# Optimization experiments

Hardware: AMD Instinct MI355X
Metric: run time of the kernel (lower is better)

Reference implementation:

```python
import jax, jax.numpy as jnp
import numpy as np

EMBED_DIM = 1024
NUM_HEADS = 16
HEAD_DIM = EMBED_DIM // NUM_HEADS


def setup_inputs() -> dict:
    key = jax.random.key(0)
    ks = jax.random.split(key, 8)
    B, S, D = 2, 2048, EMBED_DIM
    scale = 1.0 / np.sqrt(D)
    return {
        "query": jax.random.normal(ks[0], (B, S, D), dtype=jnp.float32),
        "key": jax.random.normal(ks[1], (B, S, D), dtype=jnp.float32),
        "value": jax.random.normal(ks[2], (B, S, D), dtype=jnp.float32),
        "Wq": jax.random.normal(ks[3], (D, D), dtype=jnp.float32) * scale,
        "Wk": jax.random.normal(ks[4], (D, D), dtype=jnp.float32) * scale,
        "Wv": jax.random.normal(ks[5], (D, D), dtype=jnp.float32) * scale,
        "Wo": jax.random.normal(ks[6], (D, D), dtype=jnp.float32) * scale,
        "attention_mask": jax.random.randint(ks[7], (B, S), 0, 2, dtype=jnp.int32),
    }


def reference(query, key, value, Wq, Wk, Wv, Wo, attention_mask):
    B, Sq, D = query.shape
    Sk = key.shape[1]
    H, hd = NUM_HEADS, HEAD_DIM
    # linear projections (no bias), split into heads: [B, H, S, hd]
    q = (query @ Wq).reshape(B, Sq, H, hd).transpose(0, 2, 1, 3)
    k = (key @ Wk).reshape(B, Sk, H, hd).transpose(0, 2, 1, 3)
    v = (value @ Wv).reshape(B, Sk, H, hd).transpose(0, 2, 1, 3)
    # scaled dot-product scores: [B, H, Sq, Sk]; scale uses head_dim (post-split key dim)
    scores = jnp.einsum("bhqd,bhkd->bhqk", q, k) / jnp.sqrt(jnp.float32(hd))
    # padding mask [B, Sk] broadcast to [B, 1, 1, Sk]; 0 -> -inf
    mask = attention_mask[:, None, None, :]
    scores = jnp.where(mask == 0, -jnp.inf, scores)
    weights = jax.nn.softmax(scores, axis=-1)
    out = jnp.einsum("bhqk,bhkd->bhqd", weights, v)  # [B, H, Sq, hd]
    out = out.transpose(0, 2, 1, 3).reshape(B, Sq, D)
    return out @ Wo
```

## Files before the change

### kernel.cpp

```cpp
#include <hip/hip_runtime.h>
#include <hip/hip_bf16.h>

typedef short bf16x8 __attribute__((ext_vector_type(8)));
typedef float f32x4 __attribute__((ext_vector_type(4)));

#define S_LEN 2048
#define NHEAD 16
#define DM 1024

#if __has_builtin(__builtin_amdgcn_exp2f)
#define EXP2(x) __builtin_amdgcn_exp2f(x)
#else
#define EXP2(x) exp2f(x)
#endif

__device__ __forceinline__ short f2bf(float f) {
  union { float f; unsigned u; } x; x.f = f;
  unsigned r = x.u + 0x7fffu + ((x.u >> 16) & 1u);
  return (short)(r >> 16);
}

__device__ __forceinline__ void gload16(const void* g, void* l) {
  __builtin_amdgcn_global_load_lds(
      (const __attribute__((address_space(1))) void*)g,
      (__attribute__((address_space(3))) void*)l, 16, 0, 0);
}

__global__ __launch_bounds__(256) void wtrans(const float* __restrict__ Wq, const float* __restrict__ Wk,
                                              const float* __restrict__ Wv, const float* __restrict__ Wo,
                                              short* Tq, short* Tk, short* Tv, short* To) {
  const int z = blockIdx.z;
  const float* W = (z == 0) ? Wq : (z == 1) ? Wk : (z == 2) ? Wv : Wo;
  short* T = (z == 0) ? Tq : (z == 1) ? Tk : (z == 2) ? Tv : To;
  __shared__ short Tl[64][72];
  const int tid = threadIdx.x;
  const int k0 = blockIdx.x * 64, n0 = blockIdx.y * 64;
  const int r = tid >> 2, c0 = (tid & 3) * 16;
#pragma unroll
  for (int j = 0; j < 4; j++) {
    float4 v = *(const float4*)&W[(size_t)(k0 + r) * DM + n0 + c0 + 4 * j];
    Tl[r][c0 + 4 * j + 0] = f2bf(v.x);
    Tl[r][c0 + 4 * j + 1] = f2bf(v.y);
    Tl[r][c0 + 4 * j + 2] = f2bf(v.z);
    Tl[r][c0 + 4 * j + 3] = f2bf(v.w);
  }
  __syncthreads();
  bf16x8 o0, o1;
#pragma unroll
  for (int j = 0; j < 8; j++) { o0[j] = Tl[c0 + j][r]; o1[j] = Tl[c0 + 8 + j][r]; }
  *(bf16x8*)&T[(size_t)(n0 + r) * DM + k0 + c0] = o0;
  *(bf16x8*)&T[(size_t)(n0 + r) * DM + k0 + c0 + 8] = o1;
}

__global__ __launch_bounds__(256) void xcvt(const float* __restrict__ q, const float* __restrict__ k,
                                            const float* __restrict__ v,
                                            short* xq, short* xk, short* xv) {
  const int z = blockIdx.y;
  const float* src = (z == 0) ? q : (z == 1) ? k : v;
  short* dst = (z == 0) ? xq : (z == 1) ? xk : xv;
  const size_t base = ((size_t)blockIdx.x * 256 + threadIdx.x) * 16;
  float4 a = *(const float4*)&src[base];
  float4 b = *(const float4*)&src[base + 4];
  float4 c = *(const float4*)&src[base + 8];
  float4 d = *(const float4*)&src[base + 12];
  bf16x8 o0, o1;
  o0[0] = f2bf(a.x); o0[1] = f2bf(a.y); o0[2] = f2bf(a.z); o0[3] = f2bf(a.w);
  o0[4] = f2bf(b.x); o0[5] = f2bf(b.y); o0[6] = f2bf(b.z); o0[7] = f2bf(b.w);
  o1[0] = f2bf(c.x); o1[1] = f2bf(c.y); o1[2] = f2bf(c.z); o1[3] = f2bf(c.w);
  o1[4] = f2bf(d.x); o1[5] = f2bf(d.y); o1[6] = f2bf(d.z); o1[7] = f2bf(d.w);
  *(bf16x8*)&dst[base] = o0;
  *(bf16x8*)&dst[base + 8] = o1;
}

template<int CM>
__global__ __launch_bounds__(256) void gemm3(const short* __restrict__ A, const short* __restrict__ Bt,
                                             void* __restrict__ Cp, int M, int N, int K) {
  __shared__ __align__(16) short Al[2][128 * 64];
  __shared__ __align__(16) short Bl[2][64 * 64];
  const int tid = threadIdx.x;
  const int lane = tid & 63, w = tid >> 6;
  const int wm = w >> 1, wn = w & 1;
  const int lr = lane & 15, g = lane >> 4;
  const int m0 = blockIdx.y * 128, n0 = blockIdx.x * 64;

  f32x4 acc[4][2];
#pragma unroll
  for (int i = 0; i < 4; i++)
#pragma unroll
    for (int j = 0; j < 2; j++) acc[i][j] = (f32x4){0.f, 0.f, 0.f, 0.f};

  const int srow = lane >> 3;
  const int sch = (lane & 7) ^ (srow & 7);
  const short* gA = A + (size_t)(m0 + w * 32 + srow) * K + 8 * sch;
  const short* gB = Bt + (size_t)(n0 + w * 16 + srow) * K + 8 * sch;

#define STAGE(buf, kk)                                                              \
  do {                                                                              \
    _Pragma("unroll") for (int c = 0; c < 4; c++)                                   \
        gload16(gA + (size_t)c * 8 * K + (kk), &Al[buf][(w * 32 + c * 8) * 64]);    \
    _Pragma("unroll") for (int c = 0; c < 2; c++)                                   \
        gload16(gB + (size_t)c * 8 * K + (kk), &Bl[buf][(w * 16 + c * 8) * 64]);    \
  } while (0)

  const int nsteps = K >> 6;
  STAGE(0, 0);
  int buf = 0;
  for (int t = 0; t < nsteps; t++) {
    __syncthreads();
    if (t + 1 < nsteps) STAGE(buf ^ 1, (t + 1) << 6);
#pragma unroll
    for (int kc = 0; kc < 2; kc++) {
      bf16x8 af[4], bfr[2];
#pragma unroll
      for (int mt = 0; mt < 4; mt++) {
        int row = wm * 64 + mt * 16 + lr;
        af[mt] = *(const bf16x8*)&Al[buf][row * 64 + 8 * ((kc * 4 + g) ^ (lr & 7))];
      }
#pragma unroll
      for (int nt = 0; nt < 2; nt++) {
        int row = wn * 32 + nt * 16 + lr;
        bfr[nt] = *(const bf16x8*)&Bl[buf][row * 64 + 8 * ((kc * 4 + g) ^ (lr & 7))];
      }
      __builtin_amdgcn_s_setprio(1);
#pragma unroll
      for (int mt = 0; mt < 4; mt++)
#pragma unroll
        for (int nt = 0; nt < 2; nt++)
          acc[mt][nt] = __builtin_amdgcn_mfma_f32_16x16x32_bf16(af[mt], bfr[nt], acc[mt][nt], 0, 0, 0);
      __builtin_amdgcn_s_setprio(0);
    }
    buf ^= 1;
  }
#undef STAGE

#pragma unroll
  for (int mt = 0; mt < 4; mt++)
#pragma unroll
    for (int nt = 0; nt < 2; nt++)
#pragma unroll
      for (int r = 0; r < 4; r++) {
        int row = m0 + wm * 64 + mt * 16 + g * 4 + r;
        int col = n0 + wn * 32 + nt * 16 + lr;
        if (CM == 0) {
          ((float*)Cp)[(size_t)row * N + col] = acc[mt][nt][r];
        } else if (CM == 1 || CM == 3) {
          float v = (CM == 3) ? acc[mt][nt][r] * 0.18033688011f : acc[mt][nt][r];
          int b = row >> 11, s = row & (S_LEN - 1);
          int h = col >> 6, d = col & 63;
          ((short*)Cp)[(((size_t)(b * NHEAD + h)) * S_LEN + s) * 64 + d] = f2bf(v);
        } else {
          int h = row >> 6, d = row & 63;
          int b = col >> 11, s = col & (S_LEN - 1);
          ((short*)Cp)[(((size_t)(b * NHEAD + h)) * 64 + d) * S_LEN + s] = f2bf(acc[mt][nt][r]);
        }
      }
}

template<int AM, int BMODE, int CM>
__global__ __launch_bounds__(256) void gemm2(const void* __restrict__ Ap, const void* __restrict__ Bp,
                                             void* __restrict__ Cp, int M, int N, int K) {
  __shared__ __align__(16) short Al[128][72];
  __shared__ __align__(16) short Bl[64][72];
  const int tid = threadIdx.x;
  const int lane = tid & 63, w = tid >> 6;
  const int wm = w >> 1, wn = w & 1;
  const int lr = lane & 15, g = lane >> 4;
  const int m0 = blockIdx.y * 128, n0 = blockIdx.x * 64;

  f32x4 acc[4][2];
#pragma unroll
  for (int i = 0; i < 4; i++)
#pragma unroll
    for (int j = 0; j < 2; j++) acc[i][j] = (f32x4){0.f, 0.f, 0.f, 0.f};

  const int ar = tid >> 1, ac = (tid & 1) * 32;
  const int br = tid >> 2, bc = (tid & 3) * 16;

  float4 la[8]; bf16x8 la8[4];
  float4 lb[4]; bf16x8 lb8[2];

#define LOADA(kk)                                                                        \
  do {                                                                                   \
    if (AM == 0) {                                                                       \
      const float* A = (const float*)Ap;                                                 \
      _Pragma("unroll") for (int j = 0; j < 8; j++)                                      \
          la[j] = *(const float4*)&A[(size_t)(m0 + ar) * K + (kk) + ac + 4 * j];         \
    } else {                                                                             \
      const short* A = (const short*)Ap;                                                 \
      _Pragma("unroll") for (int j = 0; j < 4; j++)                                      \
          la8[j] = *(const bf16x8*)&A[(size_t)(m0 + ar) * K + (kk) + ac + 8 * j];        \
    }                                                                                    \
  } while (0)

#define LOADB(kk)                                                                        \
  do {                                                                                   \
    if (BMODE == 0) {                                                                    \
      const float* B = (const float*)Bp;                                                 \
      _Pragma("unroll") for (int j = 0; j < 4; j++)                                      \
          lb[j] = *(const float4*)&B[(size_t)(n0 + br) * K + (kk) + bc + 4 * j];         \
    } else if (BMODE == 1) {                                                             \
      const short* B = (const short*)Bp;                                                 \
      _Pragma("unroll") for (int j = 0; j < 2; j++)                                      \
          lb8[j] = *(const bf16x8*)&B[(size_t)(n0 + br) * K + (kk) + bc + 8 * j];        \
    } else {                                                                             \
      const float* B = (const float*)Bp;                                                 \
      _Pragma("unroll") for (int j = 0; j < 4; j++)                                      \
          lb[j] = *(const float4*)&B[(size_t)((kk) + br) * N + n0 + bc + 4 * j];         \
    }                                                                                    \
  } while (0)

  const int nsteps = K >> 6;
  LOADA(0); LOADB(0);

  for (int t = 0; t < nsteps; t++) {
    __syncthreads();
    if (AM == 0) {
#pragma unroll
      for (int j = 0; j < 4; j++) {
        float4 v0 = la[2 * j], v1 = la[2 * j + 1];
        bf16x8 tt;
        tt[0] = f2bf(v0.x); tt[1] = f2bf(v0.y); tt[2] = f2bf(v0.z); tt[3] = f2bf(v0.w);
        tt[4] = f2bf(v1.x); tt[5] = f2bf(v1.y); tt[6] = f2bf(v1.z); tt[7] = f2bf(v1.w);
        *(bf16x8*)&Al[ar][ac + 8 * j] = tt;
      }
    } else {
#pragma unroll
      for (int j = 0; j < 4; j++) *(bf16x8*)&Al[ar][ac + 8 * j] = la8[j];
    }
    if (BMODE == 0) {
#pragma unroll
      for (int j = 0; j < 2; j++) {
        float4 v0 = lb[2 * j], v1 = lb[2 * j + 1];
        bf16x8 tt;
        tt[0] = f2bf(v0.x); tt[1] = f2bf(v0.y); tt[2] = f2bf(v0.z); tt[3] = f2bf(v0.w);
        tt[4] = f2bf(v1.x); tt[5] = f2bf(v1.y); tt[6] = f2bf(v1.z); tt[7] = f2bf(v1.w);
        *(bf16x8*)&Bl[br][bc + 8 * j] = tt;
      }
    } else if (BMODE == 1) {
#pragma unroll
      for (int j = 0; j < 2; j++) *(bf16x8*)&Bl[br][bc + 8 * j] = lb8[j];
    } else {
#pragma unroll
      for (int j = 0; j < 4; j++) {
        float4 v = lb[j];
        Bl[bc + 4 * j + 0][br] = f2bf(v.x);
        Bl[bc + 4 * j + 1][br] = f2bf(v.y);
        Bl[bc + 4 * j + 2][br] = f2bf(v.z);
        Bl[bc + 4 * j + 3][br] = f2bf(v.w);
      }
    }
    __syncthreads();
    if (t + 1 < nsteps) { LOADA((t + 1) << 6); LOADB((t + 1) << 6); }
#pragma unroll
    for (int kc = 0; kc < 2; kc++) {
      bf16x8 af[4], bfr[2];
#pragma unroll
      for (int mt = 0; mt < 4; mt++) af[mt] = *(const bf16x8*)&Al[wm * 64 + mt * 16 + lr][kc * 32 + g * 8];
#pragma unroll
      for (int nt = 0; nt < 2; nt++) bfr[nt] = *(const bf16x8*)&Bl[wn * 32 + nt * 16 + lr][kc * 32 + g * 8];
#pragma unroll
      for (int mt = 0; mt < 4; mt++)
#pragma unroll
        for (int nt = 0; nt < 2; nt++)
          acc[mt][nt] = __builtin_amdgcn_mfma_f32_16x16x32_bf16(af[mt], bfr[nt], acc[mt][nt], 0, 0, 0);
    }
  }
#undef LOADA
#undef LOADB

#pragma unroll
  for (int mt = 0; mt < 4; mt++)
#pragma unroll
    for (int nt = 0; nt < 2; nt++)
#pragma unroll
      for (int r = 0; r < 4; r++) {
        int row = m0 + wm * 64 + mt * 16 + g * 4 + r;
        int col = n0 + wn * 32 + nt * 16 + lr;
        if (CM == 0) {
          ((float*)Cp)[(size_t)row * N + col] = acc[mt][nt][r];
        } else if (CM == 1 || CM == 3) {
          float v = (CM == 3) ? acc[mt][nt][r] * 0.18033688011f : acc[mt][nt][r];
          int b = row >> 11, s = row & (S_LEN - 1);
          int h = col >> 6, d = col & 63;
          ((short*)Cp)[(((size_t)(b * NHEAD + h)) * S_LEN + s) * 64 + d] = f2bf(v);
        } else {
          int h = row >> 6, d = row & 63;
          int b = col >> 11, s = col & (S_LEN - 1);
          ((short*)Cp)[(((size_t)(b * NHEAD + h)) * 64 + d) * S_LEN + s] = f2bf(acc[mt][nt][r]);
        }
      }
}

__global__ __launch_bounds__(256, 2) void attn4(const short* __restrict__ Qb,
                                                const short* __restrict__ Kb,
                                                const short* __restrict__ VbT,
                                                const int* __restrict__ mask,
                                                short* __restrict__ Ob) {
  __shared__ __align__(16) short Kl[2][64][64];
  __shared__ __align__(16) short Vl[2][64][64];
  __shared__ __align__(16) short Pl[4][32][64];

  const int tid = threadIdx.x;
  const int lane = tid & 63, w = tid >> 6;
  const int lr = lane & 15, g = lane >> 4;

  const int flat = blockIdx.y * gridDim.x + blockIdx.x;
  const int wid = (flat & 7) * 64 + (flat >> 3);
  const int qblk = wid & 15, bh = wid >> 4;
  const int b = bh >> 4, h = bh & 15;
  const int qbase = qblk * 128;
  const size_t hoff = (size_t)bh * S_LEN * 64;

  bf16x8 qf[2][2];
#pragma unroll
  for (int qfr = 0; qfr < 2; qfr++)
#pragma unroll
    for (int kh = 0; kh < 2; kh++)
      qf[qfr][kh] = *(const bf16x8*)&Qb[hoff + (size_t)(qbase + w * 32 + qfr * 16 + lr) * 64 + kh * 32 + g * 8];

  f32x4 o_acc[2][4];
  float lsum[2][4];
#pragma unroll
  for (int qfr = 0; qfr < 2; qfr++) {
#pragma unroll
    for (int dg = 0; dg < 4; dg++) o_acc[qfr][dg] = (f32x4){0.f, 0.f, 0.f, 0.f};
#pragma unroll
    for (int r = 0; r < 4; r++) lsum[qfr][r] = 0.f;
  }

  const int* maskb = mask + b * S_LEN;
  const int srow = lane >> 3;
  const int sch = (lane & 7) ^ (srow & 7);
  const short* gK = Kb + hoff + (size_t)(w * 16 + srow) * 64 + 8 * sch;
  const short* gV = VbT + hoff + (size_t)(w * 16 + srow) * S_LEN + 8 * sch;

#define STAGEKV(buf, kb)                                                       \
  do {                                                                         \
    _Pragma("unroll") for (int c = 0; c < 2; c++)                              \
        gload16(gK + (size_t)(kb + c * 8) * 64, &Kl[buf][w * 16 + c * 8][0]);  \
    _Pragma("unroll") for (int c = 0; c < 2; c++)                              \
        gload16(gV + (size_t)c * 8 * S_LEN + (kb), &Vl[buf][w * 16 + c * 8][0]); \
  } while (0)

  const int NT = S_LEN / 64;
  STAGEKV(0, 0);
  int buf = 0;

  for (int t = 0; t < NT; t++) {
    const int kb = t * 64;
    __syncthreads();
    if (t + 1 < NT) STAGEKV(buf ^ 1, kb + 64);

    float bias[4];
#pragma unroll
    for (int nt = 0; nt < 4; nt++) bias[nt] = maskb[kb + 16 * nt + lr] ? 0.f : -1e30f;

    bf16x8 kfr[4][2];
#pragma unroll
    for (int nt = 0; nt < 4; nt++)
#pragma unroll
      for (int kh = 0; kh < 2; kh++)
        kfr[nt][kh] = *(const bf16x8*)&Kl[buf][nt * 16 + lr][8 * ((4 * kh + g) ^ (lr & 7))];

    f32x4 s[2][4];
#pragma unroll
    for (int qfr = 0; qfr < 2; qfr++)
#pragma unroll
      for (int nt = 0; nt < 4; nt++) s[qfr][nt] = (f32x4){0.f, 0.f, 0.f, 0.f};
    __builtin_amdgcn_s_setprio(1);
#pragma unroll
    for (int qfr = 0; qfr < 2; qfr++)
#pragma unroll
      for (int nt = 0; nt < 4; nt++) {
        s[qfr][nt] = __builtin_amdgcn_mfma_f32_16x16x32_bf16(qf[qfr][0], kfr[nt][0], s[qfr][nt], 0, 0, 0);
        s[qfr][nt] = __builtin_amdgcn_mfma_f32_16x16x32_bf16(qf[qfr][1], kfr[nt][1], s[qfr][nt], 0, 0, 0);
      }
    __builtin_amdgcn_s_setprio(0);

    bf16x8 vfr[4][2];
#pragma unroll
    for (int dg = 0; dg < 4; dg++)
#pragma unroll
      for (int kh = 0; kh < 2; kh++)
        vfr[dg][kh] = *(const bf16x8*)&Vl[buf][dg * 16 + lr][8 * ((4 * kh + g) ^ (lr & 7))];

#pragma unroll
    for (int qfr = 0; qfr < 2; qfr++)
#pragma unroll
      for (int nt = 0; nt < 4; nt++)
#pragma unroll
        for (int r = 0; r < 4; r++) {
          float p = EXP2(s[qfr][nt][r] + bias[nt]);
          lsum[qfr][r] += p;
          union { float f; unsigned u; } cv; cv.f = p;
          unsigned short pb = (unsigned short)((cv.u + 0x7fffu) >> 16);
          int q = qfr * 16 + g * 4 + r;
          Pl[w][q][(16 * nt + lr) ^ ((q & 7) << 3)] = (short)pb;
        }

#pragma unroll
    for (int qfr = 0; qfr < 2; qfr++) {
      bf16x8 pf[2];
#pragma unroll
      for (int kh = 0; kh < 2; kh++)
        pf[kh] = *(const bf16x8*)&Pl[w][qfr * 16 + lr][8 * ((4 * kh + g) ^ (lr & 7))];
      __builtin_amdgcn_s_setprio(1);
#pragma unroll
      for (int dg = 0; dg < 4; dg++) {
        o_acc[qfr][dg] = __builtin_amdgcn_mfma_f32_16x16x32_bf16(pf[0], vfr[dg][0], o_acc[qfr][dg], 0, 0, 0);
        o_acc[qfr][dg] = __builtin_amdgcn_mfma_f32_16x16x32_bf16(pf[1], vfr[dg][1], o_acc[qfr][dg], 0, 0, 0);
      }
      __builtin_amdgcn_s_setprio(0);
    }
    buf ^= 1;
  }
#undef STAGEKV

#pragma unroll
  for (int qfr = 0; qfr < 2; qfr++)
#pragma unroll
    for (int r = 0; r < 4; r++) {
      float l = lsum[qfr][r];
#pragma unroll
      for (int off = 1; off < 16; off <<= 1) l += __shfl_xor(l, off);
      float inv = 1.f / l;
      int qr = qbase + w * 32 + qfr * 16 + g * 4 + r;
#pragma unroll
      for (int dg = 0; dg < 4; dg++) {
        int col = h * 64 + dg * 16 + lr;
        Ob[((size_t)b * S_LEN + qr) * DM + col] = f2bf(o_acc[qfr][dg][r] * inv);
      }
    }
}

extern "C" void kernel_launch(void* const* d_in, const int* in_sizes, int n_in,
                              void* d_out, int out_size, void* d_ws, size_t ws_size,
                              hipStream_t stream) {
  const float* query = (const float*)d_in[0];
  const float* key   = (const float*)d_in[1];
  const float* value = (const float*)d_in[2];
  const float* Wq = (const float*)d_in[3];
  const float* Wk = (const float*)d_in[4];
  const float* Wv = (const float*)d_in[5];
  const float* Wo = (const float*)d_in[6];
  const int* mask = (const int*)d_in[7];

  char* ws = (char*)d_ws;
  const size_t MB = 1 << 20;
  const bool big = ws_size >= 41 * MB;

  dim3 ag(S_LEN / 128, 2 * NHEAD);

  if (big) {
    short* xq  = (short*)(ws);
    short* xk  = (short*)(ws + 8 * MB);
    short* xv  = (short*)(ws + 16 * MB);
    short* WqT = (short*)(ws + 24 * MB);
    short* WkT = (short*)(ws + 26 * MB);
    short* WvT = (short*)(ws + 28 * MB);
    short* WoT = (short*)(ws + 30 * MB);
    short* Qb  = (short*)(ws + 32 * MB);
    short* Kb  = xq;
    short* VbT = xk;
    short* Ob  = xv;

    dim3 tgrid(16, 16, 4);
    wtrans<<<tgrid, 256, 0, stream>>>(Wq, Wk, Wv, Wo, WqT, WkT, WvT, WoT);
    dim3 cg(1024, 3);
    xcvt<<<cg, 256, 0, stream>>>(query, key, value, xq, xk, xv);

    dim3 gqk(DM / 64, (2 * S_LEN) / 128);
    gemm3<3><<<gqk, 256, 0, stream>>>(xq, WqT, Qb, 2 * S_LEN, DM, DM);
    gemm3<1><<<gqk, 256, 0, stream>>>(xk, WkT, Kb, 2 * S_LEN, DM, DM);
    dim3 gv((2 * S_LEN) / 64, DM / 128);
    gemm3<2><<<gv, 256, 0, stream>>>(WvT, xv, VbT, DM, 2 * S_LEN, DM);

    attn4<<<ag, 256, 0, stream>>>(Qb, Kb, VbT, mask, Ob);

    gemm3<0><<<gqk, 256, 0, stream>>>(Ob, WoT, (float*)d_out, 2 * S_LEN, DM, DM);
  } else {
    short* Qb  = (short*)(ws);
    short* Kb  = (short*)(ws + 8 * MB);
    short* VbT = (short*)(ws + 16 * MB);
    short* WqT = (short*)(ws + 24 * MB);
    short* WkT = (short*)(ws + 26 * MB);
    short* WvT = (short*)(ws + 28 * MB);
    short* Ob  = (short*)(ws + 24 * MB);

    dim3 tgrid(16, 16, 3);
    wtrans<<<tgrid, 256, 0, stream>>>(Wq, Wk, Wv, Wo, WqT, WkT, WvT, WqT);

    dim3 gq(DM / 64, (2 * S_LEN) / 128);
    gemm2<0, 1, 3><<<gq, 256, 0, stream>>>(query, WqT, Qb, 2 * S_LEN, DM, DM);
    gemm2<0, 1, 1><<<gq, 256, 0, stream>>>(key,   WkT, Kb, 2 * S_LEN, DM, DM);
    dim3 gv((2 * S_LEN) / 64, DM / 128);
    gemm2<1, 0, 2><<<gv, 256, 0, stream>>>(WvT, value, VbT, DM, 2 * S_LEN, DM);

    attn4<<<ag, 256, 0, stream>>>(Qb, Kb, VbT, mask, Ob);

    gemm2<1, 2, 0><<<gq, 256, 0, stream>>>(Ob, Wo, (float*)d_out, 2 * S_LEN, DM, DM);
  }
}
```

Before: 146.1 us.

## Enlarge attention query tile to 256 rows and compute transposed scores

The attention kernel now handles 256 query rows per block (64 per wave) instead of 128, so each K/V tile staged in shared memory is reused across twice as many queries, and the grid halves. Scores are computed as K·Qᵀ, which puts each lane's four accumulator values along the key dimension. That lets the softmax numerators be packed into bf16 pairs with a single hardware convert and written to LDS as 8-byte stores, with the mask read as int4 vectors. The row-sum reduction shrinks to two shuffles. In exchange the kernel uses more registers and LDS and drops the 2-blocks-per-CU launch bound, so occupancy may fall and there are only 256 blocks to fill the device.

```diff
diff --git a/kernel.cpp b/kernel.cpp
--- a/kernel.cpp
+++ b/kernel.cpp
@@ -18,6 +18,12 @@
   union { float f; unsigned u; } x; x.f = f;
   unsigned r = x.u + 0x7fffu + ((x.u >> 16) & 1u);
   return (short)(r >> 16);
+}
+
+__device__ __forceinline__ unsigned cvt_pk_bf16(float lo, float hi) {
+  unsigned r;
+  asm("v_cvt_pk_bf16_f32 %0, %1, %2" : "=v"(r) : "v"(lo), "v"(hi));
+  return r;
 }
 
 __device__ __forceinline__ void gload16(const void* g, void* l) {
@@ -291,41 +297,40 @@
       }
 }
 
-__global__ __launch_bounds__(256, 2) void attn4(const short* __restrict__ Qb,
-                                                const short* __restrict__ Kb,
-                                                const short* __restrict__ VbT,
-                                                const int* __restrict__ mask,
-                                                short* __restrict__ Ob) {
+__global__ __launch_bounds__(256) void attn5(const short* __restrict__ Qb,
+                                              const short* __restrict__ Kb,
+                                              const short* __restrict__ VbT,
+                                              const int* __restrict__ mask,
+                                              short* __restrict__ Ob) {
   __shared__ __align__(16) short Kl[2][64][64];
   __shared__ __align__(16) short Vl[2][64][64];
-  __shared__ __align__(16) short Pl[4][32][64];
+  __shared__ __align__(16) short Pl[4][64][64];
 
   const int tid = threadIdx.x;
   const int lane = tid & 63, w = tid >> 6;
   const int lr = lane & 15, g = lane >> 4;
 
   const int flat = blockIdx.y * gridDim.x + blockIdx.x;
-  const int wid = (flat & 7) * 64 + (flat >> 3);
-  const int qblk = wid & 15, bh = wid >> 4;
+  const int wid = (flat & 7) * 32 + (flat >> 3);
+  const int qblk = wid & 7, bh = wid >> 3;
   const int b = bh >> 4, h = bh & 15;
-  const int qbase = qblk * 128;
+  const int qbase = qblk * 256;
   const size_t hoff = (size_t)bh * S_LEN * 64;
 
-  bf16x8 qf[2][2];
-#pragma unroll
-  for (int qfr = 0; qfr < 2; qfr++)
+  bf16x8 qf[4][2];
+#pragma unroll
+  for (int qfr = 0; qfr < 4; qfr++)
 #pragma unroll
     for (int kh = 0; kh < 2; kh++)
-      qf[qfr][kh] = *(const bf16x8*)&Qb[hoff + (size_t)(qbase + w * 32 + qfr * 16 + lr) * 64 + kh * 32 + g * 8];
-
-  f32x4 o_acc[2][4];
-  float lsum[2][4];
-#pragma unroll
-  for (int qfr = 0; qfr < 2; qfr++) {
+      qf[qfr][kh] = *(const bf16x8*)&Qb[hoff + (size_t)(qbase + w * 64 + qfr * 16 + lr) * 64 + kh * 32 + g * 8];
+
+  f32x4 o_acc[4][4];
+  float lsum[4];
+#pragma unroll
+  for (int qfr = 0; qfr < 4; qfr++) {
+    lsum[qfr] = 0.f;
 #pragma unroll
     for (int dg = 0; dg < 4; dg++) o_acc[qfr][dg] = (f32x4){0.f, 0.f, 0.f, 0.f};
-#pragma unroll
-    for (int r = 0; r < 4; r++) lsum[qfr][r] = 0.f;
   }
 
   const int* maskb = mask + b * S_LEN;
@@ -334,11 +339,11 @@
   const short* gK = Kb + hoff + (size_t)(w * 16 + srow) * 64 + 8 * sch;
   const short* gV = VbT + hoff + (size_t)(w * 16 + srow) * S_LEN + 8 * sch;
 
-#define STAGEKV(buf, kb)                                                       \
-  do {                                                                         \
-    _Pragma("unroll") for (int c = 0; c < 2; c++)                              \
-        gload16(gK + (size_t)(kb + c * 8) * 64, &Kl[buf][w * 16 + c * 8][0]);  \
-    _Pragma("unroll") for (int c = 0; c < 2; c++)                              \
+#define STAGEKV(buf, kb)                                                         \
+  do {                                                                           \
+    _Pragma("unroll") for (int c = 0; c < 2; c++)                                \
+        gload16(gK + (size_t)(kb + c * 8) * 64, &Kl[buf][w * 16 + c * 8][0]);    \
+    _Pragma("unroll") for (int c = 0; c < 2; c++)                                \
         gload16(gV + (size_t)c * 8 * S_LEN + (kb), &Vl[buf][w * 16 + c * 8][0]); \
   } while (0)
 
@@ -351,9 +356,15 @@
     __syncthreads();
     if (t + 1 < NT) STAGEKV(buf ^ 1, kb + 64);
 
-    float bias[4];
-#pragma unroll
-    for (int nt = 0; nt < 4; nt++) bias[nt] = maskb[kb + 16 * nt + lr] ? 0.f : -1e30f;
+    float bias[4][4];
+#pragma unroll
+    for (int nt = 0; nt < 4; nt++) {
+      int4 mv = *(const int4*)&maskb[kb + nt * 16 + 4 * g];
+      bias[nt][0] = mv.x ? 0.f : -1e30f;
+      bias[nt][1] = mv.y ? 0.f : -1e30f;
+      bias[nt][2] = mv.z ? 0.f : -1e30f;
+      bias[nt][3] = mv.w ? 0.f : -1e30f;
+    }
 
     bf16x8 kfr[4][2];
 #pragma unroll
@@ -362,21 +373,6 @@
       for (int kh = 0; kh < 2; kh++)
         kfr[nt][kh] = *(const bf16x8*)&Kl[buf][nt * 16 + lr][8 * ((4 * kh + g) ^ (lr & 7))];
 
-    f32x4 s[2][4];
-#pragma unroll
-    for (int qfr = 0; qfr < 2; qfr++)
-#pragma unroll
-      for (int nt = 0; nt < 4; nt++) s[qfr][nt] = (f32x4){0.f, 0.f, 0.f, 0.f};
-    __builtin_amdgcn_s_setprio(1);
-#pragma unroll
-    for (int qfr = 0; qfr < 2; qfr++)
-#pragma unroll
-      for (int nt = 0; nt < 4; nt++) {
-        s[qfr][nt] = __builtin_amdgcn_mfma_f32_16x16x32_bf16(qf[qfr][0], kfr[nt][0], s[qfr][nt], 0, 0, 0);
-        s[qfr][nt] = __builtin_amdgcn_mfma_f32_16x16x32_bf16(qf[qfr][1], kfr[nt][1], s[qfr][nt], 0, 0, 0);
-      }
-    __builtin_amdgcn_s_setprio(0);
-
     bf16x8 vfr[4][2];
 #pragma unroll
     for (int dg = 0; dg < 4; dg++)
@@ -385,25 +381,37 @@
         vfr[dg][kh] = *(const bf16x8*)&Vl[buf][dg * 16 + lr][8 * ((4 * kh + g) ^ (lr & 7))];
 
 #pragma unroll
-    for (int qfr = 0; qfr < 2; qfr++)
-#pragma unroll
-      for (int nt = 0; nt < 4; nt++)
-#pragma unroll
-        for (int r = 0; r < 4; r++) {
-          float p = EXP2(s[qfr][nt][r] + bias[nt]);
-          lsum[qfr][r] += p;
-          union { float f; unsigned u; } cv; cv.f = p;
-          unsigned short pb = (unsigned short)((cv.u + 0x7fffu) >> 16);
-          int q = qfr * 16 + g * 4 + r;
-          Pl[w][q][(16 * nt + lr) ^ ((q & 7) << 3)] = (short)pb;
-        }
-
-#pragma unroll
-    for (int qfr = 0; qfr < 2; qfr++) {
+    for (int qfr = 0; qfr < 4; qfr++) {
+      f32x4 s[4];
+#pragma unroll
+      for (int nt = 0; nt < 4; nt++) s[nt] = (f32x4){0.f, 0.f, 0.f, 0.f};
+      __builtin_amdgcn_s_setprio(1);
+#pragma unroll
+      for (int nt = 0; nt < 4; nt++) {
+        s[nt] = __builtin_amdgcn_mfma_f32_16x16x32_bf16(kfr[nt][0], qf[qfr][0], s[nt], 0, 0, 0);
+        s[nt] = __builtin_amdgcn_mfma_f32_16x16x32_bf16(kfr[nt][1], qf[qfr][1], s[nt], 0, 0, 0);
+      }
+      __builtin_amdgcn_s_setprio(0);
+#pragma unroll
+      for (int nt = 0; nt < 4; nt++) {
+        float p0 = EXP2(s[nt][0] + bias[nt][0]);
+        float p1 = EXP2(s[nt][1] + bias[nt][1]);
+        float p2 = EXP2(s[nt][2] + bias[nt][2]);
+        float p3 = EXP2(s[nt][3] + bias[nt][3]);
+        lsum[qfr] += (p0 + p1) + (p2 + p3);
+        uint2 pk;
+        pk.x = cvt_pk_bf16(p0, p1);
+        pk.y = cvt_pk_bf16(p2, p3);
+        *(uint2*)&Pl[w][qfr * 16 + lr][(16 * nt + 4 * g) ^ ((lr & 7) << 3)] = pk;
+      }
+    }
+
+#pragma unroll
+    for (int qfr = 0; qfr < 4; qfr++) {
       bf16x8 pf[2];
 #pragma unroll
       for (int kh = 0; kh < 2; kh++)
-        pf[kh] = *(const bf16x8*)&Pl[w][qfr * 16 + lr][8 * ((4 * kh + g) ^ (lr & 7))];
+        pf[kh] = *(const bf16x8*)&Pl[w][qfr * 16 + lr][(kh * 32 + 8 * g) ^ ((lr & 7) << 3)];
       __builtin_amdgcn_s_setprio(1);
 #pragma unroll
       for (int dg = 0; dg < 4; dg++) {
@@ -417,20 +425,23 @@
 #undef STAGEKV
 
 #pragma unroll
-  for (int qfr = 0; qfr < 2; qfr++)
-#pragma unroll
-    for (int r = 0; r < 4; r++) {
-      float l = lsum[qfr][r];
-#pragma unroll
-      for (int off = 1; off < 16; off <<= 1) l += __shfl_xor(l, off);
-      float inv = 1.f / l;
-      int qr = qbase + w * 32 + qfr * 16 + g * 4 + r;
-#pragma unroll
-      for (int dg = 0; dg < 4; dg++) {
+  for (int qfr = 0; qfr < 4; qfr++) {
+    float l = lsum[qfr];
+    l += __shfl_xor(l, 16);
+    l += __shfl_xor(l, 32);
+    float inv = 1.f / l;
+    float invq[4];
+#pragma unroll
+    for (int r = 0; r < 4; r++) invq[r] = __shfl(inv, 4 * g + r);
+#pragma unroll
+    for (int dg = 0; dg < 4; dg++)
+#pragma unroll
+      for (int r = 0; r < 4; r++) {
+        int qr = qbase + w * 64 + qfr * 16 + 4 * g + r;
         int col = h * 64 + dg * 16 + lr;
-        Ob[((size_t)b * S_LEN + qr) * DM + col] = f2bf(o_acc[qfr][dg][r] * inv);
-      }
-    }
+        Ob[((size_t)b * S_LEN + qr) * DM + col] = f2bf(o_acc[qfr][dg][r] * invq[r]);
+      }
+  }
 }
 
 extern "C" void kernel_launch(void* const* d_in, const int* in_sizes, int n_in,
@@ -449,7 +460,7 @@
   const size_t MB = 1 << 20;
   const bool big = ws_size >= 41 * MB;
 
-  dim3 ag(S_LEN / 128, 2 * NHEAD);
+  dim3 ag(S_LEN / 256, 2 * NHEAD);
 
   if (big) {
     short* xq  = (short*)(ws);
@@ -475,7 +486,7 @@
     dim3 gv((2 * S_LEN) / 64, DM / 128);
     gemm3<2><<<gv, 256, 0, stream>>>(WvT, xv, VbT, DM, 2 * S_LEN, DM);
 
-    attn4<<<ag, 256, 0, stream>>>(Qb, Kb, VbT, mask, Ob);
+    attn5<<<ag, 256, 0, stream>>>(Qb, Kb, VbT, mask, Ob);
 
     gemm3<0><<<gqk, 256, 0, stream>>>(Ob, WoT, (float*)d_out, 2 * S_LEN, DM, DM);
   } else {
@@ -496,7 +507,7 @@
     dim3 gv((2 * S_LEN) / 64, DM / 128);
     gemm2<1, 0, 2><<<gv, 256, 0, stream>>>(WvT, value, VbT, DM, 2 * S_LEN, DM);
 
-    attn4<<<ag, 256, 0, stream>>>(Qb, Kb, VbT, mask, Ob);
+    attn5<<<ag, 256, 0, stream>>>(Qb, Kb, VbT, mask, Ob);
 
     gemm2<1, 2, 0><<<gq, 256, 0, stream>>>(Ob, Wo, (float*)d_out, 2 * S_LEN, DM, DM);
   }
```

After: 164.5 us. 12.5% more time.
